# Kernel optimization log

Measured on AMD Instinct MI355X. Metric: run time of the kernel, lower is better.

## Reference

```python
import jax, jax.numpy as jnp
import numpy as np

TEMPERATURE = 0.05
EPS = 1e-12  # F.normalize eps


def _l2norm(x):
    n = jnp.sqrt(jnp.sum(x * x, axis=-1, keepdims=True))
    return x / jnp.maximum(n, EPS)


def setup_inputs() -> dict:
    key = jax.random.key(0)
    k1, k2, k3 = jax.random.split(key, 3)
    B, S, D = 8, 1536, 1024
    h1 = jax.random.normal(k1, (B, S, D), dtype=jnp.float32)
    h2 = jax.random.normal(k2, (B, S, D), dtype=jnp.float32)
    mask = jax.random.randint(k3, (B, S), 0, 2).astype(bool)
    return {"last_hidden_states_1": h1, "last_hidden_states_2": h2, "token_mask_batch": mask}


def reference(last_hidden_states_1, last_hidden_states_2, token_mask_batch):
    # Vectorized equivalent of the per-sample python loop: padded (masked) tokens
    # simply contribute nothing to pos/neg sums or the mean.
    B, S, D = last_hidden_states_1.shape
    f1 = _l2norm(last_hidden_states_1)  # [B,S,D]
    f2 = _l2norm(last_hidden_states_2)
    feats = jnp.concatenate([f1, f2], axis=1)  # [B,2S,D]

    # positive pairs: token i in view1 vs token i in view2
    pos_sim = jnp.sum(f1 * f2, axis=-1).astype(jnp.float32) / TEMPERATURE  # [B,S]
    pos = jnp.exp(jnp.concatenate([pos_sim, pos_sim], axis=1))  # [B,2S]

    # all-pairs similarities among the 2n effective tokens
    sim = jnp.einsum("bid,bjd->bij", feats, feats).astype(jnp.float32) / TEMPERATURE  # [B,2S,2S]

    m2 = jnp.concatenate([token_mask_batch, token_mask_batch], axis=1)  # [B,2S]
    tok = jnp.arange(2 * S) % S
    same_token = tok[:, None] == tok[None, :]  # excludes self and its positive counterpart
    neg_mask = m2[:, :, None] & m2[:, None, :] & (~same_token)  # [B,2S,2S]

    Ng = jnp.sum(jnp.exp(sim) * neg_mask, axis=-1)  # [B,2S]
    per_tok = -jnp.log(pos / (Ng + pos))  # [B,2S]

    m2f = m2.astype(jnp.float32)
    per_sample = jnp.sum(per_tok * m2f, axis=1) / jnp.sum(m2f, axis=1)  # mean over 2n tokens
    return jnp.mean(per_sample)
```

## Files before the change

kernel.cpp:

```cpp
#include <hip/hip_runtime.h>
#include <hip/hip_bf16.h>
#include <math.h>

#define BATCH 8
#define SEQ   1536
#define DIM   1024
#define SEQ2  (2*SEQ)
#define TEMP_INV 20.0f
#define EXP_SCALE (TEMP_INV / 64.0f)

#define BM 128
#define BN 128
#define BK 128
#define KITERS (DIM/BK)
#define TILES  (SEQ2 / BM)
#define NPAIRS (TILES * (TILES+1) / 2)

typedef int   i32x4 __attribute__((ext_vector_type(4)));
typedef int   i32x8 __attribute__((ext_vector_type(8)));
typedef float f32x4 __attribute__((ext_vector_type(4)));

#define GLOBAL_AS __attribute__((address_space(1)))
#define LDS_AS    __attribute__((address_space(3)))

__device__ inline void async_ld16(const void* g, void* lds_uniform) {
    __builtin_amdgcn_global_load_lds((const GLOBAL_AS void*)g, (LDS_AS void*)lds_uniform, 16, 0, 0);
}

__device__ inline float wave_red64(float v) {
    #pragma unroll
    for (int m = 32; m > 0; m >>= 1) v += __shfl_xor(v, m, 64);
    return v;
}

__global__ __launch_bounds__(256) void normalize_kernel(
        const float* __restrict__ h1, const float* __restrict__ h2,
        unsigned char* __restrict__ feats, float* __restrict__ pos_cos,
        float* __restrict__ Ng) {
    int w = threadIdx.x >> 6, lane = threadIdx.x & 63;
    int tok = blockIdx.x * 4 + w;
    int b = tok / SEQ, s = tok - b * SEQ;

    const float4* a4 = (const float4*)(h1 + (size_t)tok * DIM);
    const float4* b4 = (const float4*)(h2 + (size_t)tok * DIM);
    float4 av[4], bv[4];
    #pragma unroll
    for (int it = 0; it < 4; it++) { av[it] = a4[lane + 64*it]; bv[it] = b4[lane + 64*it]; }

    float ss1 = 0.f, ss2 = 0.f, sd = 0.f;
    #pragma unroll
    for (int it = 0; it < 4; it++) {
        ss1 += av[it].x*av[it].x + av[it].y*av[it].y + av[it].z*av[it].z + av[it].w*av[it].w;
        ss2 += bv[it].x*bv[it].x + bv[it].y*bv[it].y + bv[it].z*bv[it].z + bv[it].w*bv[it].w;
        sd  += av[it].x*bv[it].x + av[it].y*bv[it].y + av[it].z*bv[it].z + av[it].w*bv[it].w;
    }
    ss1 = wave_red64(ss1); ss2 = wave_red64(ss2); sd = wave_red64(sd);

    float sc1 = 1.0f / fmaxf(sqrtf(ss1), 1e-12f);
    float sc2 = 1.0f / fmaxf(sqrtf(ss2), 1e-12f);
    float s18 = sc1 * 8.0f, s28 = sc2 * 8.0f;

    unsigned int* f1row = (unsigned int*)(feats + ((size_t)b * SEQ2 + s) * DIM);
    unsigned int* f2row = (unsigned int*)(feats + ((size_t)b * SEQ2 + SEQ + s) * DIM);
    #pragma unroll
    for (int it = 0; it < 4; it++) {
        int p1 = __builtin_amdgcn_cvt_pk_fp8_f32(av[it].x * s18, av[it].y * s18, 0, 0);
        p1     = __builtin_amdgcn_cvt_pk_fp8_f32(av[it].z * s18, av[it].w * s18, p1, 1);
        int p2 = __builtin_amdgcn_cvt_pk_fp8_f32(bv[it].x * s28, bv[it].y * s28, 0, 0);
        p2     = __builtin_amdgcn_cvt_pk_fp8_f32(bv[it].z * s28, bv[it].w * s28, p2, 1);
        f1row[lane + 64*it] = (unsigned int)p1;
        f2row[lane + 64*it] = (unsigned int)p2;
    }
    if (lane == 0) {
        pos_cos[tok] = sd * sc1 * sc2;
        Ng[2*tok] = 0.0f;
        Ng[2*tok + 1] = 0.0f;
    }
}

__global__ __launch_bounds__(256) void gemm_ng_kernel(
        const unsigned char* __restrict__ feats, const int* __restrict__ mask,
        float* __restrict__ Ng) {
    int b = blockIdx.z;
    int p = blockIdx.x;
    int ti = 0;
    while (p >= TILES - ti) { p -= TILES - ti; ti++; }
    int tj = ti + p;
    int ibase = ti * BM, jbase = tj * BN;
    bool isdiag = (ti == tj);

    const unsigned char* fb = feats + (size_t)b * SEQ2 * DIM;

    __shared__ __align__(16) unsigned char As[BM][BK];
    __shared__ __align__(16) unsigned char Bs[BN][BK];
    __shared__ float mrow_s[BM];
    __shared__ float mcol_s[BN];

    int t = threadIdx.x;
    int lane = t & 63, w = t >> 6;
    int wrow = w >> 1, wcol = w & 1;
    int colq = lane & 15, quad = lane >> 4;

    if (t < BM) {
        int i = ibase + t; int im = (i < SEQ) ? i : i - SEQ;
        mrow_s[t] = mask[b * SEQ + im] ? 1.0f : 0.0f;
    } else {
        int j = jbase + (t - BM); int jm = (j < SEQ) ? j : j - SEQ;
        mcol_s[t - BM] = mask[b * SEQ + jm] ? 1.0f : 0.0f;
    }

    int sr = t >> 3;
    int sc = (t & 7) ^ (sr & 7);
    const unsigned char* a0 = fb + (size_t)(ibase + sr) * DIM + sc * 16;
    const unsigned char* b0 = fb + (size_t)(jbase + sr) * DIM + sc * 16;

    f32x4 acc[4][4] = {};
    int s0 = ((2 * quad)     ^ (colq & 7)) * 16;
    int s1 = ((2 * quad + 1) ^ (colq & 7)) * 16;

    for (int it = 0; it < KITERS; it++) {
        __syncthreads();
        size_t kb = (size_t)it * BK;
        #pragma unroll
        for (int q = 0; q < 4; q++) {
            async_ld16(a0 + (size_t)q * 32 * DIM + kb, (char*)&As[0][0] + q * 4096 + w * 1024);
            async_ld16(b0 + (size_t)q * 32 * DIM + kb, (char*)&Bs[0][0] + q * 4096 + w * 1024);
        }
        asm volatile("s_waitcnt vmcnt(0)" ::: "memory");
        __syncthreads();

        i32x8 af[4], bg[4];
        #pragma unroll
        for (int mi = 0; mi < 4; mi++) {
            int row = wrow * 64 + mi * 16 + colq;
            i32x4 lo = *(const i32x4*)&As[row][s0];
            i32x4 hi = *(const i32x4*)&As[row][s1];
            af[mi] = __builtin_shufflevector(lo, hi, 0, 1, 2, 3, 4, 5, 6, 7);
        }
        #pragma unroll
        for (int nj = 0; nj < 4; nj++) {
            int row = wcol * 64 + nj * 16 + colq;
            i32x4 lo = *(const i32x4*)&Bs[row][s0];
            i32x4 hi = *(const i32x4*)&Bs[row][s1];
            bg[nj] = __builtin_shufflevector(lo, hi, 0, 1, 2, 3, 4, 5, 6, 7);
        }

        #pragma unroll
        for (int mi = 0; mi < 4; mi++)
            #pragma unroll
            for (int nj = 0; nj < 4; nj++)
                acc[mi][nj] = __builtin_amdgcn_mfma_scale_f32_16x16x128_f8f6f4(
                    af[mi], bg[nj], acc[mi][nj],
                    0, 0,
                    0, 0x7F7F7F7F,
                    0, 0x7F7F7F7F);
    }

    float mj[4]; int jglob[4];
    #pragma unroll
    for (int nj = 0; nj < 4; nj++) {
        int jl = wcol * 64 + nj * 16 + colq;
        mj[nj] = mcol_s[jl];
        jglob[nj] = jbase + jl;
    }
    float colsum[4] = {0.f, 0.f, 0.f, 0.f};

    #pragma unroll
    for (int mi = 0; mi < 4; mi++) {
        int il0 = wrow * 64 + mi * 16 + quad * 4;
        float rsum[4] = {0.f, 0.f, 0.f, 0.f};
        float mr[4];
        #pragma unroll
        for (int r = 0; r < 4; r++) mr[r] = mrow_s[il0 + r];
        #pragma unroll
        for (int nj = 0; nj < 4; nj++) {
            #pragma unroll
            for (int r = 0; r < 4; r++) {
                int d = (ibase + il0 + r) - jglob[nj];
                bool same = (d == 0) | (d == SEQ) | (d == -SEQ);
                float e = same ? 0.0f : __expf(acc[mi][nj][r] * EXP_SCALE);
                rsum[r] += e * mj[nj];
                colsum[nj] += e * mr[r];
            }
        }
        #pragma unroll
        for (int r = 0; r < 4; r++) {
            float v = rsum[r];
            #pragma unroll
            for (int m = 1; m < 16; m <<= 1) v += __shfl_xor(v, m, 64);
            if (colq == 0)
                atomicAdd(&Ng[b * SEQ2 + ibase + il0 + r], v);
        }
    }

    if (!isdiag) {
        #pragma unroll
        for (int nj = 0; nj < 4; nj++) {
            float v = colsum[nj];
            v += __shfl_xor(v, 16, 64);
            v += __shfl_xor(v, 32, 64);
            if (quad == 0)
                atomicAdd(&Ng[b * SEQ2 + jglob[nj]], v);
        }
    }
}

__global__ __launch_bounds__(256) void loss_kernel(
        const float* __restrict__ Ng, const float* __restrict__ pos_cos,
        const int* __restrict__ mask, float* __restrict__ per_sample) {
    int b = blockIdx.x, t = threadIdx.x;
    float sum = 0.f, cnt = 0.f;
    for (int i = t; i < SEQ2; i += 256) {
        int im = (i < SEQ) ? i : i - SEQ;
        if (mask[b * SEQ + im]) {
            float ps = pos_cos[b * SEQ + im] * TEMP_INV;
            float ng = Ng[b * SEQ2 + i];
            sum += log1pf(ng * __expf(-ps));
            cnt += 1.0f;
        }
    }
    sum = wave_red64(sum); cnt = wave_red64(cnt);
    __shared__ float rs[4], rc[4];
    int lane = t & 63, w = t >> 6;
    if (lane == 0) { rs[w] = sum; rc[w] = cnt; }
    __syncthreads();
    if (t == 0) {
        float s = rs[0]+rs[1]+rs[2]+rs[3];
        float c = rc[0]+rc[1]+rc[2]+rc[3];
        per_sample[b] = s / c;
    }
}

__global__ void final_kernel(const float* __restrict__ per_sample, float* __restrict__ out) {
    if (threadIdx.x == 0) {
        float s = 0.f;
        #pragma unroll
        for (int b = 0; b < BATCH; b++) s += per_sample[b];
        out[0] = s / (float)BATCH;
    }
}

extern "C" void kernel_launch(void* const* d_in, const int* in_sizes, int n_in,
                              void* d_out, int out_size, void* d_ws, size_t ws_size,
                              hipStream_t stream) {
    const float* h1  = (const float*)d_in[0];
    const float* h2  = (const float*)d_in[1];
    const int* mask  = (const int*)d_in[2];
    float* out       = (float*)d_out;

    char* ws = (char*)d_ws;
    size_t feats_bytes = (size_t)BATCH * SEQ2 * DIM;
    unsigned char* feats = (unsigned char*)ws;
    float* pos_cos    = (float*)(ws + feats_bytes);
    float* Ng         = (float*)(ws + feats_bytes + (size_t)BATCH * SEQ * 4);
    float* per_sample = (float*)(ws + feats_bytes + (size_t)BATCH * SEQ * 4
                                 + (size_t)BATCH * SEQ2 * 4);

    normalize_kernel<<<BATCH * SEQ / 4, 256, 0, stream>>>(h1, h2, feats, pos_cos, Ng);

    dim3 g2(NPAIRS, 1, BATCH);
    gemm_ng_kernel<<<g2, 256, 0, stream>>>(feats, mask, Ng);

    loss_kernel<<<BATCH, 256, 0, stream>>>(Ng, pos_cos, mask, per_sample);
    final_kernel<<<1, 64, 0, stream>>>(per_sample, out);
}
```

Before: 218.4 us.

## Give each wave private LDS tiles and prefetch next K slice without barriers

Each wave now loads its own 64-row A and B slices into a private LDS region, so the block-wide __syncthreads around every K iteration are gone. The next K slice is issued asynchronously after the current fragments are read into registers, so loads overlap the MFMA work. The mask values are read straight from global memory instead of staged in shared memory. In exchange each wave loads its own copy of rows that were previously shared within the block, which doubles global/L2 traffic per block and raises LDS use to 64KB, which may lower occupancy.

```diff
diff --git a/kernel.cpp b/kernel.cpp
--- a/kernel.cpp
+++ b/kernel.cpp
@@ -91,59 +91,56 @@
 
     const unsigned char* fb = feats + (size_t)b * SEQ2 * DIM;
 
-    __shared__ __align__(16) unsigned char As[BM][BK];
-    __shared__ __align__(16) unsigned char Bs[BN][BK];
-    __shared__ float mrow_s[BM];
-    __shared__ float mcol_s[BN];
+    __shared__ __align__(16) unsigned char lds[4][16384];
 
     int t = threadIdx.x;
     int lane = t & 63, w = t >> 6;
     int wrow = w >> 1, wcol = w & 1;
     int colq = lane & 15, quad = lane >> 4;
 
-    if (t < BM) {
-        int i = ibase + t; int im = (i < SEQ) ? i : i - SEQ;
-        mrow_s[t] = mask[b * SEQ + im] ? 1.0f : 0.0f;
-    } else {
-        int j = jbase + (t - BM); int jm = (j < SEQ) ? j : j - SEQ;
-        mcol_s[t - BM] = mask[b * SEQ + jm] ? 1.0f : 0.0f;
-    }
-
-    int sr = t >> 3;
-    int sc = (t & 7) ^ (sr & 7);
-    const unsigned char* a0 = fb + (size_t)(ibase + sr) * DIM + sc * 16;
-    const unsigned char* b0 = fb + (size_t)(jbase + sr) * DIM + sc * 16;
+    unsigned char* myA = &lds[w][0];
+    unsigned char* myB = &lds[w][8192];
+
+    int lr = lane >> 3;
+    int sc = (lane & 7) ^ lr;
+    const unsigned char* pa = fb + (size_t)(ibase + wrow * 64 + lr) * DIM + sc * 16;
+    const unsigned char* pb = fb + (size_t)(jbase + wcol * 64 + lr) * DIM + sc * 16;
+
+    auto stage = [&](int kb) {
+        #pragma unroll
+        for (int q = 0; q < 8; q++) {
+            async_ld16(pa + (size_t)q * 8 * DIM + kb, myA + q * 1024);
+            async_ld16(pb + (size_t)q * 8 * DIM + kb, myB + q * 1024);
+        }
+    };
 
     f32x4 acc[4][4] = {};
     int s0 = ((2 * quad)     ^ (colq & 7)) * 16;
     int s1 = ((2 * quad + 1) ^ (colq & 7)) * 16;
 
+    stage(0);
+
+    #pragma unroll 1
     for (int it = 0; it < KITERS; it++) {
-        __syncthreads();
-        size_t kb = (size_t)it * BK;
-        #pragma unroll
-        for (int q = 0; q < 4; q++) {
-            async_ld16(a0 + (size_t)q * 32 * DIM + kb, (char*)&As[0][0] + q * 4096 + w * 1024);
-            async_ld16(b0 + (size_t)q * 32 * DIM + kb, (char*)&Bs[0][0] + q * 4096 + w * 1024);
-        }
         asm volatile("s_waitcnt vmcnt(0)" ::: "memory");
-        __syncthreads();
 
         i32x8 af[4], bg[4];
         #pragma unroll
         for (int mi = 0; mi < 4; mi++) {
-            int row = wrow * 64 + mi * 16 + colq;
-            i32x4 lo = *(const i32x4*)&As[row][s0];
-            i32x4 hi = *(const i32x4*)&As[row][s1];
+            int row = mi * 16 + colq;
+            i32x4 lo = *(const i32x4*)(myA + row * 128 + s0);
+            i32x4 hi = *(const i32x4*)(myA + row * 128 + s1);
             af[mi] = __builtin_shufflevector(lo, hi, 0, 1, 2, 3, 4, 5, 6, 7);
         }
         #pragma unroll
         for (int nj = 0; nj < 4; nj++) {
-            int row = wcol * 64 + nj * 16 + colq;
-            i32x4 lo = *(const i32x4*)&Bs[row][s0];
-            i32x4 hi = *(const i32x4*)&Bs[row][s1];
+            int row = nj * 16 + colq;
+            i32x4 lo = *(const i32x4*)(myB + row * 128 + s0);
+            i32x4 hi = *(const i32x4*)(myB + row * 128 + s1);
             bg[nj] = __builtin_shufflevector(lo, hi, 0, 1, 2, 3, 4, 5, 6, 7);
         }
+        asm volatile("s_waitcnt lgkmcnt(0)" ::: "memory");
+        if (it + 1 < KITERS) stage((it + 1) * BK);
 
         #pragma unroll
         for (int mi = 0; mi < 4; mi++)
@@ -156,12 +153,14 @@
                     0, 0x7F7F7F7F);
     }
 
+    const int* mb = mask + b * SEQ;
     float mj[4]; int jglob[4];
     #pragma unroll
     for (int nj = 0; nj < 4; nj++) {
-        int jl = wcol * 64 + nj * 16 + colq;
-        mj[nj] = mcol_s[jl];
-        jglob[nj] = jbase + jl;
+        int j = jbase + wcol * 64 + nj * 16 + colq;
+        int jm = (j < SEQ) ? j : j - SEQ;
+        mj[nj] = mb[jm] ? 1.0f : 0.0f;
+        jglob[nj] = j;
     }
     float colsum[4] = {0.f, 0.f, 0.f, 0.f};
 
@@ -171,7 +170,11 @@
         float rsum[4] = {0.f, 0.f, 0.f, 0.f};
         float mr[4];
         #pragma unroll
-        for (int r = 0; r < 4; r++) mr[r] = mrow_s[il0 + r];
+        for (int r = 0; r < 4; r++) {
+            int i = ibase + il0 + r;
+            int im = (i < SEQ) ? i : i - SEQ;
+            mr[r] = mb[im] ? 1.0f : 0.0f;
+        }
         #pragma unroll
         for (int nj = 0; nj < 4; nj++) {
             #pragma unroll
```

New measurement: 225.4 us. 3.2% more time.
